# Optimization experiments

Measured on AMD Instinct MI355X. Metric: run time of the kernel, lower is better.

The kernel has to match this reference:

```python
import jax, jax.numpy as jnp
import numpy as np

NUM_CLUSTERS = 1024
FEATURE_SIZE = 512
EPS_NORM = 1e-12   # torch F.normalize eps
EPS_P = 1e-16      # entropy clamp


def _l2_normalize(a):
    n = jnp.sqrt(jnp.sum(a * a, axis=-1, keepdims=True))
    return a / jnp.maximum(n, EPS_NORM)


def setup_inputs() -> dict:
    key = jax.random.key(0)
    kx, km = jax.random.split(key)
    x = jax.random.normal(kx, (65536, FEATURE_SIZE), dtype=jnp.float32)
    # cluster-center parameter (original uses SVD-orthonormal rows; any float
    # init is equivalent math-wise since rows are re-normalized in forward)
    m = jax.random.normal(km, (NUM_CLUSTERS, FEATURE_SIZE), dtype=jnp.float32)
    return {"x": x, "m": m}


def reference(x, m):
    # cosine-similarity logits: [N, K]
    y = jnp.einsum('nf,kf->nk', _l2_normalize(x), _l2_normalize(m))
    p = jax.nn.softmax(y, axis=-1)
    # clamp into (0, 1) exactly as the torch code does
    p = jnp.where(p <= 0, EPS_P, p)
    p = jnp.where(p >= 1, 1.0 - EPS_P, p)
    # shannon entropy per row, then mean
    ent = -jnp.sum(p * jnp.log(p), axis=-1)  # [N]
    intra = jnp.mean(ent)
    inter = jnp.float32(0.0)
    total = intra
    return (total, intra, inter)
```

## Files before the change

### kernel.cpp

```cpp
#include <hip/hip_runtime.h>
#include <hip/hip_bf16.h>

typedef __bf16 bf16x8 __attribute__((ext_vector_type(8)));
typedef float  f32x4  __attribute__((ext_vector_type(4)));

#define N_ROWS 65536
#define N_CLU  1024
#define N_F    512

__device__ __forceinline__ void gload_lds16(const void* g, void* l) {
  __builtin_amdgcn_global_load_lds(
      (const __attribute__((address_space(1))) void*)g,
      (__attribute__((address_space(3))) void*)l, 16, 0, 0);
}

__global__ __launch_bounds__(256) void knorm_m(const float* __restrict__ m,
                                               __bf16* __restrict__ mn) {
  const int wave = threadIdx.x >> 6, lane = threadIdx.x & 63;
  const int row = blockIdx.x * 4 + wave;
  const float* p = m + (size_t)row * N_F + lane * 8;
  float4 a = ((const float4*)p)[0];
  float4 b = ((const float4*)p)[1];
  float ss = a.x*a.x + a.y*a.y + a.z*a.z + a.w*a.w
           + b.x*b.x + b.y*b.y + b.z*b.z + b.w*b.w;
#pragma unroll
  for (int off = 1; off < 64; off <<= 1) ss += __shfl_xor(ss, off);
  const float inv = 1.0f / fmaxf(sqrtf(ss), 1e-12f);
  bf16x8 o;
  o[0] = (__bf16)(a.x*inv); o[1] = (__bf16)(a.y*inv);
  o[2] = (__bf16)(a.z*inv); o[3] = (__bf16)(a.w*inv);
  o[4] = (__bf16)(b.x*inv); o[5] = (__bf16)(b.y*inv);
  o[6] = (__bf16)(b.z*inv); o[7] = (__bf16)(b.w*inv);
  *(bf16x8*)(mn + (size_t)row * N_F + lane * 8) = o;
}

__global__ __launch_bounds__(256, 2) void kmain(const float* __restrict__ x,
                                                const __bf16* __restrict__ mn,
                                                float* __restrict__ acc_out) {
  __shared__ __align__(16) __bf16 mbuf[2][32][520];
  const int tid = threadIdx.x, wave = tid >> 6, lane = tid & 63;
  const int r16 = lane & 15, g = lane >> 4;

#pragma unroll
  for (int k = 0; k < 8; ++k) {
    const int r = wave * 8 + k;
    gload_lds16((const char*)mn + (size_t)r * (N_F * 2) + lane * 16,
                &mbuf[0][r][0]);
  }

  bf16x8 xf0[16], xf1[16];
  const int row0 = blockIdx.x * 128 + wave * 32;
  {
    const float* p0 = x + (size_t)(row0 + r16) * N_F + g * 8;
    float ss = 0.f;
#pragma unroll
    for (int i = 0; i < 16; ++i) {
      float4 a = *(const float4*)(p0 + i * 32);
      float4 b = *(const float4*)(p0 + i * 32 + 4);
      ss += a.x*a.x + a.y*a.y + a.z*a.z + a.w*a.w
          + b.x*b.x + b.y*b.y + b.z*b.z + b.w*b.w;
      bf16x8 f;
      f[0] = (__bf16)a.x; f[1] = (__bf16)a.y; f[2] = (__bf16)a.z; f[3] = (__bf16)a.w;
      f[4] = (__bf16)b.x; f[5] = (__bf16)b.y; f[6] = (__bf16)b.z; f[7] = (__bf16)b.w;
      xf0[i] = f;
    }
    ss += __shfl_xor(ss, 16); ss += __shfl_xor(ss, 32);
    const float inv = 1.0f / fmaxf(sqrtf(ss), 1e-12f);
#pragma unroll
    for (int i = 0; i < 16; ++i)
#pragma unroll
      for (int j = 0; j < 8; ++j)
        xf0[i][j] = (__bf16)((float)xf0[i][j] * inv);
  }
  {
    const float* p1 = x + (size_t)(row0 + 16 + r16) * N_F + g * 8;
    float ss = 0.f;
#pragma unroll
    for (int i = 0; i < 16; ++i) {
      float4 a = *(const float4*)(p1 + i * 32);
      float4 b = *(const float4*)(p1 + i * 32 + 4);
      ss += a.x*a.x + a.y*a.y + a.z*a.z + a.w*a.w
          + b.x*b.x + b.y*b.y + b.z*b.z + b.w*b.w;
      bf16x8 f;
      f[0] = (__bf16)a.x; f[1] = (__bf16)a.y; f[2] = (__bf16)a.z; f[3] = (__bf16)a.w;
      f[4] = (__bf16)b.x; f[5] = (__bf16)b.y; f[6] = (__bf16)b.z; f[7] = (__bf16)b.w;
      xf1[i] = f;
    }
    ss += __shfl_xor(ss, 16); ss += __shfl_xor(ss, 32);
    const float inv = 1.0f / fmaxf(sqrtf(ss), 1e-12f);
#pragma unroll
    for (int i = 0; i < 16; ++i)
#pragma unroll
      for (int j = 0; j < 8; ++j)
        xf1[i][j] = (__bf16)((float)xf1[i][j] * inv);
  }

  float L0 = 0.f, L1 = 0.f, S0 = 0.f, S1 = 0.f;
  __syncthreads();

  for (int t = 0; t < 32; ++t) {
    const int cur = t & 1;
    if (t < 31) {
#pragma unroll
      for (int k = 0; k < 8; ++k) {
        const int r = wave * 8 + k;
        const int c = (t + 1) * 32 + r;
        gload_lds16((const char*)mn + (size_t)c * (N_F * 2) + lane * 16,
                    &mbuf[cur ^ 1][r][0]);
      }
    }
    f32x4 a00 = {0,0,0,0}, a01 = {0,0,0,0}, a10 = {0,0,0,0}, a11 = {0,0,0,0};
    const __bf16* mb0 = &mbuf[cur][r16][g * 8];
    const __bf16* mb1 = &mbuf[cur][16 + r16][g * 8];
#pragma unroll
    for (int i = 0; i < 16; ++i) {
      bf16x8 a0 = *(const bf16x8*)(mb0 + i * 32);
      bf16x8 a1 = *(const bf16x8*)(mb1 + i * 32);
      a00 = __builtin_amdgcn_mfma_f32_16x16x32_bf16(a0, xf0[i], a00, 0, 0, 0);
      a01 = __builtin_amdgcn_mfma_f32_16x16x32_bf16(a0, xf1[i], a01, 0, 0, 0);
      a10 = __builtin_amdgcn_mfma_f32_16x16x32_bf16(a1, xf0[i], a10, 0, 0, 0);
      a11 = __builtin_amdgcn_mfma_f32_16x16x32_bf16(a1, xf1[i], a11, 0, 0, 0);
    }
#pragma unroll
    for (int r = 0; r < 4; ++r) {
      { float y = a00[r]; float e = __expf(y); L0 += e; S0 = fmaf(e, y, S0); }
      { float y = a10[r]; float e = __expf(y); L0 += e; S0 = fmaf(e, y, S0); }
      { float y = a01[r]; float e = __expf(y); L1 += e; S1 = fmaf(e, y, S1); }
      { float y = a11[r]; float e = __expf(y); L1 += e; S1 = fmaf(e, y, S1); }
    }
    __syncthreads();
  }

  float h = 0.f;
  {
    float L = L0; L += __shfl_xor(L, 16); L += __shfl_xor(L, 32);
    float S = S0; S += __shfl_xor(S, 16); S += __shfl_xor(S, 32);
    h += __logf(L) - S / L;
  }
  {
    float L = L1; L += __shfl_xor(L, 16); L += __shfl_xor(L, 32);
    float S = S1; S += __shfl_xor(S, 16); S += __shfl_xor(S, 32);
    h += __logf(L) - S / L;
  }
  h *= 0.25f;
#pragma unroll
  for (int off = 1; off < 64; off <<= 1) h += __shfl_xor(h, off);
  if (lane == 0) atomicAdd(acc_out, h);
}

__global__ void kfin(const float* __restrict__ acc, float* __restrict__ out) {
  const float mean = acc[0] * (1.0f / (float)N_ROWS);
  out[0] = mean;
  out[1] = mean;
  out[2] = 0.0f;
}

extern "C" void kernel_launch(void* const* d_in, const int* in_sizes, int n_in,
                              void* d_out, int out_size, void* d_ws, size_t ws_size,
                              hipStream_t stream) {
  const float* x = (const float*)d_in[0];
  const float* m = (const float*)d_in[1];
  float* acc = (float*)d_ws;
  __bf16* mn = (__bf16*)((char*)d_ws + 64);

  hipMemsetAsync(d_ws, 0, 64, stream);
  knorm_m<<<256, 256, 0, stream>>>(m, mn);
  kmain<<<512, 256, 0, stream>>>(x, mn, acc);
  kfin<<<1, 1, 0, stream>>>(acc, (float*)d_out);
}
```

Measured before the change: 101.2 us.

## Switch GEMM operands to FP8 with swizzled triple-buffered LDS pipeline

Normalized x and m are now quantized to FP8 and multiplied with fp8 MFMA instructions instead of bf16. This halves the cluster-matrix bytes and LDS traffic. Cluster tiles are staged through registers into a 3-deep XOR-swizzled LDS ring rather than direct global-to-LDS loads, using explicit waitcnt and barrier. The x normalization pass now reads x twice, once for the norm and once to quantize, rather than keeping bf16 copies. FP8 precision risks reduced accuracy in the cosine logits and the entropy.

```diff
diff --git a/kernel.cpp b/kernel.cpp
--- a/kernel.cpp
+++ b/kernel.cpp
@@ -1,21 +1,20 @@
 #include <hip/hip_runtime.h>
 #include <hip/hip_bf16.h>
 
-typedef __bf16 bf16x8 __attribute__((ext_vector_type(8)));
 typedef float  f32x4  __attribute__((ext_vector_type(4)));
+typedef unsigned long long u64;
 
 #define N_ROWS 65536
+#define N_F    512
 #define N_CLU  1024
-#define N_F    512
 
-__device__ __forceinline__ void gload_lds16(const void* g, void* l) {
-  __builtin_amdgcn_global_load_lds(
-      (const __attribute__((address_space(1))) void*)g,
-      (__attribute__((address_space(3))) void*)l, 16, 0, 0);
+template <bool HI>
+static __device__ __forceinline__ unsigned pk8(float a, float b, unsigned old) {
+  return (unsigned)__builtin_amdgcn_cvt_pk_fp8_f32(a, b, (int)old, HI);
 }
 
 __global__ __launch_bounds__(256) void knorm_m(const float* __restrict__ m,
-                                               __bf16* __restrict__ mn) {
+                                               uint2* __restrict__ mn) {
   const int wave = threadIdx.x >> 6, lane = threadIdx.x & 63;
   const int row = blockIdx.x * 4 + wave;
   const float* p = m + (size_t)row * N_F + lane * 8;
@@ -26,100 +25,54 @@
 #pragma unroll
   for (int off = 1; off < 64; off <<= 1) ss += __shfl_xor(ss, off);
   const float inv = 1.0f / fmaxf(sqrtf(ss), 1e-12f);
-  bf16x8 o;
-  o[0] = (__bf16)(a.x*inv); o[1] = (__bf16)(a.y*inv);
-  o[2] = (__bf16)(a.z*inv); o[3] = (__bf16)(a.w*inv);
-  o[4] = (__bf16)(b.x*inv); o[5] = (__bf16)(b.y*inv);
-  o[6] = (__bf16)(b.z*inv); o[7] = (__bf16)(b.w*inv);
-  *(bf16x8*)(mn + (size_t)row * N_F + lane * 8) = o;
+  unsigned lo = pk8<false>(a.x*inv, a.y*inv, 0u);
+  lo = pk8<true>(a.z*inv, a.w*inv, lo);
+  unsigned hi = pk8<false>(b.x*inv, b.y*inv, 0u);
+  hi = pk8<true>(b.z*inv, b.w*inv, hi);
+  mn[(size_t)row * 64 + lane] = make_uint2(lo, hi);
 }
 
 __global__ __launch_bounds__(256, 2) void kmain(const float* __restrict__ x,
-                                                const __bf16* __restrict__ mn,
+                                                const u64* __restrict__ mn8,
                                                 float* __restrict__ acc_out) {
-  __shared__ __align__(16) __bf16 mbuf[2][32][520];
+  __shared__ u64 mbuf[3][32][64];
   const int tid = threadIdx.x, wave = tid >> 6, lane = tid & 63;
   const int r16 = lane & 15, g = lane >> 4;
 
+  long xb0[16], xb1[16];
+  float L0 = 0.f, S0 = 0.f, L1 = 0.f, S1 = 0.f;
+
+  auto loadset = [&](u64* s, int t) {
+    const char* base = (const char*)mn8 + ((size_t)(t * 32 + wave * 8) << 9) + lane * 8;
 #pragma unroll
-  for (int k = 0; k < 8; ++k) {
-    const int r = wave * 8 + k;
-    gload_lds16((const char*)mn + (size_t)r * (N_F * 2) + lane * 16,
-                &mbuf[0][r][0]);
-  }
+    for (int k = 0; k < 8; ++k) s[k] = *(const u64*)(base + (k << 9));
+  };
+  const int lxw = lane ^ ((wave & 1) << 3);
+  auto writeset = [&](const u64* s, int t) {
+    char* dst = (char*)&mbuf[t % 3][wave * 8][0];
+#pragma unroll
+    for (int k = 0; k < 8; ++k)
+      *(u64*)(dst + (k << 9) + ((lxw ^ k) << 3)) = s[k];
+  };
 
-  bf16x8 xf0[16], xf1[16];
-  const int row0 = blockIdx.x * 128 + wave * 32;
-  {
-    const float* p0 = x + (size_t)(row0 + r16) * N_F + g * 8;
-    float ss = 0.f;
+  const int swzhi = (r16 & 12) << 3;
+  const int boff0 = (r16 << 9) + ((g ^ (r16 & 3)) << 3);
+
+  auto tile = [&](int t) {
+    const char* mb = (const char*)&mbuf[t % 3][0][0];
+    const char* b0 = mb + boff0;
+    const char* b1 = b0 + (16 << 9);
+    f32x4 a00 = {0.f,0.f,0.f,0.f}, a01 = {0.f,0.f,0.f,0.f};
+    f32x4 a10 = {0.f,0.f,0.f,0.f}, a11 = {0.f,0.f,0.f,0.f};
 #pragma unroll
     for (int i = 0; i < 16; ++i) {
-      float4 a = *(const float4*)(p0 + i * 32);
-      float4 b = *(const float4*)(p0 + i * 32 + 4);
-      ss += a.x*a.x + a.y*a.y + a.z*a.z + a.w*a.w
-          + b.x*b.x + b.y*b.y + b.z*b.z + b.w*b.w;
-      bf16x8 f;
-      f[0] = (__bf16)a.x; f[1] = (__bf16)a.y; f[2] = (__bf16)a.z; f[3] = (__bf16)a.w;
-      f[4] = (__bf16)b.x; f[5] = (__bf16)b.y; f[6] = (__bf16)b.z; f[7] = (__bf16)b.w;
-      xf0[i] = f;
-    }
-    ss += __shfl_xor(ss, 16); ss += __shfl_xor(ss, 32);
-    const float inv = 1.0f / fmaxf(sqrtf(ss), 1e-12f);
-#pragma unroll
-    for (int i = 0; i < 16; ++i)
-#pragma unroll
-      for (int j = 0; j < 8; ++j)
-        xf0[i][j] = (__bf16)((float)xf0[i][j] * inv);
-  }
-  {
-    const float* p1 = x + (size_t)(row0 + 16 + r16) * N_F + g * 8;
-    float ss = 0.f;
-#pragma unroll
-    for (int i = 0; i < 16; ++i) {
-      float4 a = *(const float4*)(p1 + i * 32);
-      float4 b = *(const float4*)(p1 + i * 32 + 4);
-      ss += a.x*a.x + a.y*a.y + a.z*a.z + a.w*a.w
-          + b.x*b.x + b.y*b.y + b.z*b.z + b.w*b.w;
-      bf16x8 f;
-      f[0] = (__bf16)a.x; f[1] = (__bf16)a.y; f[2] = (__bf16)a.z; f[3] = (__bf16)a.w;
-      f[4] = (__bf16)b.x; f[5] = (__bf16)b.y; f[6] = (__bf16)b.z; f[7] = (__bf16)b.w;
-      xf1[i] = f;
-    }
-    ss += __shfl_xor(ss, 16); ss += __shfl_xor(ss, 32);
-    const float inv = 1.0f / fmaxf(sqrtf(ss), 1e-12f);
-#pragma unroll
-    for (int i = 0; i < 16; ++i)
-#pragma unroll
-      for (int j = 0; j < 8; ++j)
-        xf1[i][j] = (__bf16)((float)xf1[i][j] * inv);
-  }
-
-  float L0 = 0.f, L1 = 0.f, S0 = 0.f, S1 = 0.f;
-  __syncthreads();
-
-  for (int t = 0; t < 32; ++t) {
-    const int cur = t & 1;
-    if (t < 31) {
-#pragma unroll
-      for (int k = 0; k < 8; ++k) {
-        const int r = wave * 8 + k;
-        const int c = (t + 1) * 32 + r;
-        gload_lds16((const char*)mn + (size_t)c * (N_F * 2) + lane * 16,
-                    &mbuf[cur ^ 1][r][0]);
-      }
-    }
-    f32x4 a00 = {0,0,0,0}, a01 = {0,0,0,0}, a10 = {0,0,0,0}, a11 = {0,0,0,0};
-    const __bf16* mb0 = &mbuf[cur][r16][g * 8];
-    const __bf16* mb1 = &mbuf[cur][16 + r16][g * 8];
-#pragma unroll
-    for (int i = 0; i < 16; ++i) {
-      bf16x8 a0 = *(const bf16x8*)(mb0 + i * 32);
-      bf16x8 a1 = *(const bf16x8*)(mb1 + i * 32);
-      a00 = __builtin_amdgcn_mfma_f32_16x16x32_bf16(a0, xf0[i], a00, 0, 0, 0);
-      a01 = __builtin_amdgcn_mfma_f32_16x16x32_bf16(a0, xf1[i], a01, 0, 0, 0);
-      a10 = __builtin_amdgcn_mfma_f32_16x16x32_bf16(a1, xf0[i], a10, 0, 0, 0);
-      a11 = __builtin_amdgcn_mfma_f32_16x16x32_bf16(a1, xf1[i], a11, 0, 0, 0);
+      const int off = (i << 5) ^ swzhi;
+      long a0 = *(const long*)(b0 + off);
+      long a1 = *(const long*)(b1 + off);
+      a00 = __builtin_amdgcn_mfma_f32_16x16x32_fp8_fp8(a0, xb0[i], a00, 0, 0, 0);
+      a01 = __builtin_amdgcn_mfma_f32_16x16x32_fp8_fp8(a0, xb1[i], a01, 0, 0, 0);
+      a10 = __builtin_amdgcn_mfma_f32_16x16x32_fp8_fp8(a1, xb0[i], a10, 0, 0, 0);
+      a11 = __builtin_amdgcn_mfma_f32_16x16x32_fp8_fp8(a1, xb1[i], a11, 0, 0, 0);
     }
 #pragma unroll
     for (int r = 0; r < 4; ++r) {
@@ -128,7 +81,68 @@
       { float y = a01[r]; float e = __expf(y); L1 += e; S1 = fmaf(e, y, S1); }
       { float y = a11[r]; float e = __expf(y); L1 += e; S1 = fmaf(e, y, S1); }
     }
-    __syncthreads();
+  };
+
+  u64 sA[8], sB[8];
+  loadset(sA, 0);
+  loadset(sB, 1);
+
+  const int row0 = blockIdx.x * 128 + wave * 32;
+  const float* px0 = x + (size_t)(row0 + r16) * N_F + g * 8;
+  const float* px1 = x + (size_t)(row0 + 16 + r16) * N_F + g * 8;
+  float ss0 = 0.f, ss1 = 0.f;
+#pragma unroll
+  for (int i = 0; i < 16; ++i) {
+    float4 a = *(const float4*)(px0 + i * 32);
+    float4 b = *(const float4*)(px0 + i * 32 + 4);
+    ss0 += a.x*a.x + a.y*a.y + a.z*a.z + a.w*a.w
+         + b.x*b.x + b.y*b.y + b.z*b.z + b.w*b.w;
+    float4 c = *(const float4*)(px1 + i * 32);
+    float4 d = *(const float4*)(px1 + i * 32 + 4);
+    ss1 += c.x*c.x + c.y*c.y + c.z*c.z + c.w*c.w
+         + d.x*d.x + d.y*d.y + d.z*d.z + d.w*d.w;
+  }
+  ss0 += __shfl_xor(ss0, 16); ss0 += __shfl_xor(ss0, 32);
+  ss1 += __shfl_xor(ss1, 16); ss1 += __shfl_xor(ss1, 32);
+  const float inv0 = 1.0f / fmaxf(sqrtf(ss0), 1e-12f);
+  const float inv1 = 1.0f / fmaxf(sqrtf(ss1), 1e-12f);
+
+#pragma unroll
+  for (int i = 0; i < 16; ++i) {
+    float4 a = *(const float4*)(px0 + i * 32);
+    float4 b = *(const float4*)(px0 + i * 32 + 4);
+    unsigned lo = pk8<false>(a.x*inv0, a.y*inv0, 0u);
+    lo = pk8<true>(a.z*inv0, a.w*inv0, lo);
+    unsigned hi = pk8<false>(b.x*inv0, b.y*inv0, 0u);
+    hi = pk8<true>(b.z*inv0, b.w*inv0, hi);
+    xb0[i] = (long)(((u64)hi << 32) | lo);
+    float4 c = *(const float4*)(px1 + i * 32);
+    float4 d = *(const float4*)(px1 + i * 32 + 4);
+    unsigned lo1 = pk8<false>(c.x*inv1, c.y*inv1, 0u);
+    lo1 = pk8<true>(c.z*inv1, c.w*inv1, lo1);
+    unsigned hi1 = pk8<false>(d.x*inv1, d.y*inv1, 0u);
+    hi1 = pk8<true>(d.z*inv1, d.w*inv1, hi1);
+    xb1[i] = (long)(((u64)hi1 << 32) | lo1);
+  }
+
+  writeset(sA, 0);
+  writeset(sB, 1);
+  loadset(sA, 2);
+  asm volatile("s_waitcnt lgkmcnt(0)" ::: "memory");
+  __builtin_amdgcn_s_barrier();
+
+#pragma unroll 1
+  for (int t = 0; t < 32; t += 2) {
+    if (t + 2 < 32) writeset(sA, t + 2);
+    if (t + 3 < 32) loadset(sB, t + 3);
+    tile(t);
+    asm volatile("s_waitcnt lgkmcnt(0)" ::: "memory");
+    __builtin_amdgcn_s_barrier();
+    if (t + 3 < 32) writeset(sB, t + 3);
+    if (t + 4 < 32) loadset(sA, t + 4);
+    tile(t + 1);
+    asm volatile("s_waitcnt lgkmcnt(0)" ::: "memory");
+    __builtin_amdgcn_s_barrier();
   }
 
   float h = 0.f;
@@ -161,10 +175,10 @@
   const float* x = (const float*)d_in[0];
   const float* m = (const float*)d_in[1];
   float* acc = (float*)d_ws;
-  __bf16* mn = (__bf16*)((char*)d_ws + 64);
+  uint2* mn = (uint2*)((char*)d_ws + 64);
 
-  hipMemsetAsync(d_ws, 0, 64, stream);
+  (void)hipMemsetAsync(d_ws, 0, 64, stream);
   knorm_m<<<256, 256, 0, stream>>>(m, mn);
-  kmain<<<512, 256, 0, stream>>>(x, mn, acc);
+  kmain<<<512, 256, 0, stream>>>(x, (const u64*)mn, acc);
   kfin<<<1, 1, 0, stream>>>(acc, (float*)d_out);
 }
```

Result: faster. 98.89 us (-2.2%).
